# Performance work log

Measured on AMD Instinct MI355X. Metric: run time of the kernel, lower is better.

## Reference

```python
import jax, jax.numpy as jnp
import numpy as np
import math

N, S, E, H = 32, 64, 512, 4
HD = E // H
EQ = E // 4
L2_TEMP = 13.544
LN_EPS = 1e-5


def _ln(x, g, b):
    m = jnp.mean(x, -1, keepdims=True)
    v = jnp.var(x, -1, keepdims=True)
    return (x - m) * jax.lax.rsqrt(v + LN_EPS) * g + b


def setup_inputs() -> dict:
    key = jax.random.key(0)
    ks = jax.random.split(key, 16)
    sc = 0.02
    inp = {
        "x": jax.random.normal(ks[0], (N, S, E), jnp.float32),
        # MultiheadAttention params (torch layout: in_proj_weight (3E,E))
        "Wqkv": jax.random.normal(ks[1], (3 * E, E), jnp.float32) * sc,
        "bqkv": jnp.zeros((3 * E,), jnp.float32),
        "Wo": jax.random.normal(ks[2], (E, E), jnp.float32) * sc,
        "bo": jnp.zeros((E,), jnp.float32),
        # fc1 (E, 2E), fc2 (E, E)
        "W1": jax.random.normal(ks[3], (E, 2 * E), jnp.float32) * sc,
        "b1": jnp.zeros((E,), jnp.float32),
        "W2": jax.random.normal(ks[4], (E, E), jnp.float32) * sc,
        "b2": jnp.zeros((E,), jnp.float32),
        # layer norms
        "g1": jnp.ones((E,), jnp.float32), "be1": jnp.zeros((E,), jnp.float32),
        "g2": jnp.ones((E,), jnp.float32), "be2": jnp.zeros((E,), jnp.float32),
        # fc_diff1: Linear(E, E//4), Linear(E//4, 1)
        "d1W1": jax.random.normal(ks[5], (EQ, E), jnp.float32) * sc,
        "d1b1": jnp.zeros((EQ,), jnp.float32),
        "d1W2": jax.random.normal(ks[6], (1, EQ), jnp.float32) * sc,
        "d1b2": jnp.zeros((1,), jnp.float32),
        # fc_diff2
        "d2W1": jax.random.normal(ks[7], (EQ, E), jnp.float32) * sc,
        "d2b1": jnp.zeros((EQ,), jnp.float32),
        "d2W2": jax.random.normal(ks[8], (1, EQ), jnp.float32) * sc,
        "d2b2": jnp.zeros((1,), jnp.float32),
    }
    return inp


def _mha(x, Wqkv, bqkv, Wo, bo):
    n, s, e = x.shape
    qkv = x @ Wqkv.T + bqkv
    q, k, v = jnp.split(qkv, 3, axis=-1)
    sh = lambda t: t.reshape(n, s, H, HD).transpose(0, 2, 1, 3)  # (n,H,s,hd)
    q, k, v = sh(q), sh(k), sh(v)
    scores = jnp.einsum('bhqd,bhkd->bhqk', q, k) / math.sqrt(HD)
    a = jax.nn.softmax(scores, axis=-1)
    o = jnp.einsum('bhqk,bhkd->bhqd', a, v).transpose(0, 2, 1, 3).reshape(n, s, e)
    return o @ Wo.T + bo, a.mean(axis=1)  # averaged attn weights (torch default)


def _pair_mlp(diff_w, W1a, b1a, W2a, b2a):
    # F.relu applied after every 'layer' (Linear, Dropout(eval=id), Linear)
    h = jax.nn.relu(diff_w @ W1a.T + b1a)  # relu(dropout(relu)) == relu composed -> same
    return jax.nn.relu(h @ W2a.T + b2a)[..., 0]  # (N,f,f)


def reference(x, Wqkv, bqkv, Wo, bo, W1, b1, W2, b2, g1, be1, g2, be2,
              d1W1, d1b1, d1W2, d1b2, d2W1, d2b1, d2W2, d2b2):
    # diff[b,f,g,e] = x[b,g,e] - x[b,f,e]
    diff = x[:, None, :, :] - x[:, :, None, :]  # (N,f,f,E)
    x1_attn = jax.nn.softmax(-jnp.sum(diff * diff, -1) / L2_TEMP, axis=-1)  # (N,f,f)
    x1 = jnp.einsum('bfg,bge->bfe', x1_attn, x)
    x2, x2_attn = _mha(x, Wqkv, bqkv, Wo, bo)
    x_res = jnp.concatenate([x1, x2], axis=-1)
    h = x + jax.nn.relu(x_res @ W1.T + b1)  # dropout eval = identity
    h = _ln(h, g1, be1)
    h = h + jax.nn.relu(h @ W2.T + b2)
    out = _ln(h, g2, be2)
    diff1 = _pair_mlp(diff * x1_attn[..., None], d1W1, d1b1, d1W2, d1b2)
    diff2 = _pair_mlp(diff * x2_attn[..., None], d2W1, d2b1, d2W2, d2b2)
    return out, x1_attn[:, None], x2_attn[:, None], diff1, diff2
```

## Files before the change

### kernel.cpp

```cpp
#include <hip/hip_runtime.h>
#include <math.h>

#define NB 32
#define SS 64
#define EE 512
#define L2T 13.544f
#define LNEPS 1e-5f

using bf16x8 = __attribute__((ext_vector_type(8))) __bf16;
using u16x8  = __attribute__((ext_vector_type(8))) unsigned short;
using f32x4  = __attribute__((ext_vector_type(4))) float;

typedef const void __attribute__((address_space(1))) cv_global;
typedef void __attribute__((address_space(3))) v_lds;

__device__ inline unsigned short f2bf(float f) {
    union { float f; unsigned u; } v; v.f = f;
    unsigned r = v.u + 0x7fff + ((v.u >> 16) & 1);
    return (unsigned short)(r >> 16);
}
__device__ inline float bf2f(unsigned short h) {
    union { unsigned u; float f; } v; v.u = (unsigned)h << 16;
    return v.f;
}

__global__ __launch_bounds__(256)
void convert_all(const float* __restrict__ x, const float* __restrict__ Wqkv,
                 const float* __restrict__ Wo, const float* __restrict__ W1,
                 const float* __restrict__ W2, const float* __restrict__ d1,
                 const float* __restrict__ d2, unsigned short* __restrict__ dst) {
    int i = blockIdx.x * 256 + threadIdx.x;
    const float* s; int off;
    if (i < 1048576)      { s = x;    off = 0; }
    else if (i < 1835008) { s = Wqkv; off = 1048576; }
    else if (i < 2097152) { s = Wo;   off = 1835008; }
    else if (i < 2621440) { s = W1;   off = 2097152; }
    else if (i < 2883584) { s = W2;   off = 2621440; }
    else if (i < 2949120) { s = d1;   off = 2883584; }
    else                  { s = d2;   off = 2949120; }
    dst[i] = f2bf(s[i - off]);
}

__global__ __launch_bounds__(256)
void l2attn_x1(const float* __restrict__ x, float* __restrict__ x1_attn,
               unsigned short* __restrict__ x_resb) {
    const int f = blockIdx.x, b = blockIdx.y;
    const int tid = threadIdx.x, wave = tid >> 6, lane = tid & 63;
    __shared__ float d2s[64];
    __shared__ float attn_s[64];

    const float4* xb = (const float4*)(x + (size_t)b * SS * EE);
    float4 xf0 = xb[f * 128 + lane * 2];
    float4 xf1 = xb[f * 128 + lane * 2 + 1];

    for (int g = wave; g < 64; g += 4) {
        float4 a0 = xb[g * 128 + lane * 2];
        float4 a1 = xb[g * 128 + lane * 2 + 1];
        float dx, s = 0.f;
        dx = a0.x - xf0.x; s += dx * dx;
        dx = a0.y - xf0.y; s += dx * dx;
        dx = a0.z - xf0.z; s += dx * dx;
        dx = a0.w - xf0.w; s += dx * dx;
        dx = a1.x - xf1.x; s += dx * dx;
        dx = a1.y - xf1.y; s += dx * dx;
        dx = a1.z - xf1.z; s += dx * dx;
        dx = a1.w - xf1.w; s += dx * dx;
        #pragma unroll
        for (int m = 32; m; m >>= 1) s += __shfl_xor(s, m);
        if (lane == 0) d2s[g] = s;
    }
    __syncthreads();

    if (tid < 64) {
        float v = -d2s[tid] * (1.0f / L2T);
        float mx = v;
        #pragma unroll
        for (int m = 32; m; m >>= 1) mx = fmaxf(mx, __shfl_xor(mx, m));
        float e = expf(v - mx);
        float sum = e;
        #pragma unroll
        for (int m = 32; m; m >>= 1) sum += __shfl_xor(sum, m);
        float a = e / sum;
        x1_attn[((size_t)b * SS + f) * SS + tid] = a;
        attn_s[tid] = a;
    }
    __syncthreads();

    const float* xbf = x + (size_t)b * SS * EE;
    float acc0 = 0.f, acc1 = 0.f;
    #pragma unroll 8
    for (int g = 0; g < 64; ++g) {
        float ag = attn_s[g];
        acc0 += ag * xbf[g * EE + tid];
        acc1 += ag * xbf[g * EE + tid + 256];
    }
    unsigned short* dst = x_resb + ((size_t)b * SS + f) * 1024;
    dst[tid] = f2bf(acc0);
    dst[tid + 256] = f2bf(acc1);
}

template <bool RELU, bool OUTBF16>
__global__ __launch_bounds__(256)
void gemm_mfma(const unsigned short* __restrict__ A, int lda,
               const unsigned short* __restrict__ B, int ldb,
               const float* __restrict__ bias, float* __restrict__ Cf,
               unsigned short* __restrict__ Cb, int ldc, int K) {
    __shared__ unsigned short Asl[64 * 32];
    __shared__ unsigned short Bsl[64 * 32];
    const int tid = threadIdx.x;
    const int wave = tid >> 6, lane = tid & 63;
    const int m0 = blockIdx.y * 64, n0 = blockIdx.x * 64;
    const int wm = (wave >> 1) * 32, wn = (wave & 1) * 32;

    f32x4 acc00 = {0.f, 0.f, 0.f, 0.f};
    f32x4 acc01 = acc00, acc10 = acc00, acc11 = acc00;

    const int srow = tid >> 2, scol = (tid & 3) * 8;
    const unsigned short* Ag = A + (size_t)(m0 + srow) * lda + scol;
    const unsigned short* Bg = B + (size_t)(n0 + srow) * ldb + scol;
    v_lds* AslW = (v_lds*)(Asl + wave * 512);
    v_lds* BslW = (v_lds*)(Bsl + wave * 512);

    const int fr = lane & 15;
    const int kq = (lane >> 4) * 8;

    for (int k0 = 0; k0 < K; k0 += 32) {
        __builtin_amdgcn_global_load_lds((cv_global*)(Ag + k0), AslW, 16, 0, 0);
        __builtin_amdgcn_global_load_lds((cv_global*)(Bg + k0), BslW, 16, 0, 0);
        __syncthreads();
        bf16x8 a0 = *(const bf16x8*)(Asl + (wm + fr) * 32 + kq);
        bf16x8 a1 = *(const bf16x8*)(Asl + (wm + 16 + fr) * 32 + kq);
        bf16x8 b0 = *(const bf16x8*)(Bsl + (wn + fr) * 32 + kq);
        bf16x8 b1 = *(const bf16x8*)(Bsl + (wn + 16 + fr) * 32 + kq);
        acc00 = __builtin_amdgcn_mfma_f32_16x16x32_bf16(a0, b0, acc00, 0, 0, 0);
        acc01 = __builtin_amdgcn_mfma_f32_16x16x32_bf16(a0, b1, acc01, 0, 0, 0);
        acc10 = __builtin_amdgcn_mfma_f32_16x16x32_bf16(a1, b0, acc10, 0, 0, 0);
        acc11 = __builtin_amdgcn_mfma_f32_16x16x32_bf16(a1, b1, acc11, 0, 0, 0);
        __syncthreads();
    }

    const int crow = (lane >> 4) * 4, ccol = lane & 15;
    float bj0 = bias ? bias[n0 + wn + ccol] : 0.f;
    float bj1 = bias ? bias[n0 + wn + 16 + ccol] : 0.f;

    auto store_tile = [&](f32x4 acc, int mt, int nt, float bj) {
        #pragma unroll
        for (int r = 0; r < 4; ++r) {
            size_t m = (size_t)(m0 + mt + crow + r);
            int n = n0 + nt + ccol;
            float v = acc[r] + bj;
            if (RELU) v = fmaxf(v, 0.f);
            if (OUTBF16) Cb[m * ldc + n] = f2bf(v);
            else         Cf[m * ldc + n] = v;
        }
    };
    store_tile(acc00, wm,      wn,      bj0);
    store_tile(acc01, wm,      wn + 16, bj1);
    store_tile(acc10, wm + 16, wn,      bj0);
    store_tile(acc11, wm + 16, wn + 16, bj1);
}

__global__ __launch_bounds__(256)
void mha_attn(const unsigned short* __restrict__ qkv,
              unsigned short* __restrict__ o_buf, float* __restrict__ x2_attn) {
    const int hh = blockIdx.x;
    const int h = hh >> 1, half = hh & 1;
    const int b = blockIdx.y;
    const int tid = threadIdx.x, wave = tid >> 6, lane = tid & 63;

    __shared__ unsigned short Qs[32 * 136];
    __shared__ unsigned short Ks[64 * 136];
    __shared__ unsigned short Vt[128 * 72];
    __shared__ float sc[32 * 68];
    __shared__ unsigned short Pb[32 * 72];

    const unsigned short* base = qkv + (size_t)b * 64 * 1536;

    {
        int row = tid >> 3, col = (tid & 7) * 16;
        const unsigned short* src = base + (half * 32 + row) * 1536 + h * 128 + col;
        *(u16x8*)(Qs + row * 136 + col)     = *(const u16x8*)(src);
        *(u16x8*)(Qs + row * 136 + col + 8) = *(const u16x8*)(src + 8);
    }
    {
        int row = tid >> 2, col = (tid & 3) * 32;
        const unsigned short* src = base + row * 1536 + 512 + h * 128 + col;
        #pragma unroll
        for (int j = 0; j < 4; ++j)
            *(u16x8*)(Ks + row * 136 + col + j * 8) = *(const u16x8*)(src + j * 8);
    }
    {
        int g = tid >> 2, col = (tid & 3) * 32;
        const unsigned short* src = base + g * 1536 + 1024 + h * 128 + col;
        #pragma unroll
        for (int j = 0; j < 4; ++j) {
            u16x8 v = *(const u16x8*)(src + j * 8);
            #pragma unroll
            for (int e = 0; e < 8; ++e)
                Vt[(col + j * 8 + e) * 72 + g] = v[e];
        }
    }
    __syncthreads();

    const int fr = lane & 15, kq = (lane >> 4) * 8;
    const int crow = (lane >> 4) * 4, ccol = lane & 15;
    const int wm = (wave >> 1) * 16;

    {
        const int wn = (wave & 1) * 32;
        f32x4 s0 = {0.f, 0.f, 0.f, 0.f}, s1 = s0;
        #pragma unroll
        for (int k0 = 0; k0 < 128; k0 += 32) {
            bf16x8 a  = *(const bf16x8*)(Qs + (wm + fr) * 136 + k0 + kq);
            bf16x8 b0 = *(const bf16x8*)(Ks + (wn + fr) * 136 + k0 + kq);
            bf16x8 b1 = *(const bf16x8*)(Ks + (wn + 16 + fr) * 136 + k0 + kq);
            s0 = __builtin_amdgcn_mfma_f32_16x16x32_bf16(a, b0, s0, 0, 0, 0);
            s1 = __builtin_amdgcn_mfma_f32_16x16x32_bf16(a, b1, s1, 0, 0, 0);
        }
        const float scale = 0.08838834764831845f;
        #pragma unroll
        for (int r = 0; r < 4; ++r) {
            sc[(wm + crow + r) * 68 + wn + ccol]      = s0[r] * scale;
            sc[(wm + crow + r) * 68 + wn + 16 + ccol] = s1[r] * scale;
        }
    }
    __syncthreads();

    #pragma unroll
    for (int i = 0; i < 8; ++i) {
        int f = wave * 8 + i;
        float v = sc[f * 68 + lane];
        float mx = v;
        #pragma unroll
        for (int m = 32; m; m >>= 1) mx = fmaxf(mx, __shfl_xor(mx, m));
        float e = expf(v - mx);
        float sum = e;
        #pragma unroll
        for (int m = 32; m; m >>= 1) sum += __shfl_xor(sum, m);
        float a = e / sum;
        Pb[f * 72 + lane] = f2bf(a);
        atomicAdd(&x2_attn[((size_t)b * 64 + half * 32 + f) * 64 + lane], 0.25f * a);
    }
    __syncthreads();

    {
        const int wn2 = (wave & 1) * 64;
        f32x4 o[4];
        #pragma unroll
        for (int t = 0; t < 4; ++t) o[t] = f32x4{0.f, 0.f, 0.f, 0.f};
        #pragma unroll
        for (int k0 = 0; k0 < 64; k0 += 32) {
            bf16x8 a = *(const bf16x8*)(Pb + (wm + fr) * 72 + k0 + kq);
            #pragma unroll
            for (int t = 0; t < 4; ++t) {
                bf16x8 bv = *(const bf16x8*)(Vt + (wn2 + t * 16 + fr) * 72 + k0 + kq);
                o[t] = __builtin_amdgcn_mfma_f32_16x16x32_bf16(a, bv, o[t], 0, 0, 0);
            }
        }
        #pragma unroll
        for (int t = 0; t < 4; ++t) {
            #pragma unroll
            for (int r = 0; r < 4; ++r) {
                size_t m = (size_t)b * 64 + half * 32 + wm + crow + r;
                int col = h * 128 + wn2 + t * 16 + ccol;
                o_buf[m * 512 + col] = f2bf(o[t][r]);
            }
        }
    }
}

__global__ __launch_bounds__(256)
void add_ln(const float* __restrict__ base, const float* __restrict__ u,
            const float* __restrict__ gam, const float* __restrict__ bet,
            float* __restrict__ out, unsigned short* __restrict__ outb) {
    const int row = blockIdx.x;
    const int tid = threadIdx.x, wave = tid >> 6, lane = tid & 63;
    const float* br = base + (size_t)row * EE;
    const float* ur = u + (size_t)row * EE;
    float t0 = br[tid] + ur[tid];
    float t1 = br[tid + 256] + ur[tid + 256];
    float s = t0 + t1, sq = t0 * t0 + t1 * t1;
    #pragma unroll
    for (int m = 32; m; m >>= 1) {
        s += __shfl_xor(s, m);
        sq += __shfl_xor(sq, m);
    }
    __shared__ float ssum[4], ssq[4];
    if (lane == 0) { ssum[wave] = s; ssq[wave] = sq; }
    __syncthreads();
    s = ssum[0] + ssum[1] + ssum[2] + ssum[3];
    sq = ssq[0] + ssq[1] + ssq[2] + ssq[3];
    float mean = s * (1.0f / EE);
    float var = sq * (1.0f / EE) - mean * mean;
    float inv = rsqrtf(var + LNEPS);
    float v0 = (t0 - mean) * inv * gam[tid] + bet[tid];
    float v1 = (t1 - mean) * inv * gam[tid + 256] + bet[tid + 256];
    float* orow = out + (size_t)row * EE;
    orow[tid] = v0;
    orow[tid + 256] = v1;
    if (outb) {
        unsigned short* obr = outb + (size_t)row * EE;
        obr[tid] = f2bf(v0);
        obr[tid + 256] = f2bf(v1);
    }
}

__global__ __launch_bounds__(256)
void pair_mlp(const float* __restrict__ P, const float* __restrict__ a1,
              const float* __restrict__ a2, const float* __restrict__ d1b1,
              const float* __restrict__ d1w2, const float* __restrict__ d1b2,
              const float* __restrict__ d2b1, const float* __restrict__ d2w2,
              const float* __restrict__ d2b2, float* __restrict__ out1,
              float* __restrict__ out2) {
    const int f = blockIdx.x, b = blockIdx.y;
    const int tid = threadIdx.x, wave = tid >> 6, lane = tid & 63;
    const size_t row = (size_t)b * SS + f;
    const int c0 = lane * 2, c1 = lane * 2 + 1;

    const float p1f0 = P[row * 256 + c0],       p1f1 = P[row * 256 + c1];
    const float p2f0 = P[row * 256 + 128 + c0], p2f1 = P[row * 256 + 128 + c1];
    const float w10 = d1w2[c0], w11 = d1w2[c1];
    const float w20 = d2w2[c0], w21 = d2w2[c1];
    const float b10 = d1b1[c0], b11 = d1b1[c1];
    const float b20 = d2b1[c0], b21 = d2b1[c1];
    const float bb1 = d1b2[0], bb2 = d2b2[0];

    const float* a1r = a1 + row * SS;
    const float* a2r = a2 + row * SS;
    const size_t bbase = (size_t)b * SS * 256;

    for (int g = wave; g < 64; g += 4) {
        float aa1 = a1r[g], aa2 = a2r[g];
        float q10 = P[bbase + g * 256 + c0],       q11 = P[bbase + g * 256 + c1];
        float q20 = P[bbase + g * 256 + 128 + c0], q21 = P[bbase + g * 256 + 128 + c1];
        float h10 = fmaxf(aa1 * (q10 - p1f0) + b10, 0.f);
        float h11 = fmaxf(aa1 * (q11 - p1f1) + b11, 0.f);
        float h20 = fmaxf(aa2 * (q20 - p2f0) + b20, 0.f);
        float h21 = fmaxf(aa2 * (q21 - p2f1) + b21, 0.f);
        float s1 = w10 * h10 + w11 * h11;
        float s2 = w20 * h20 + w21 * h21;
        #pragma unroll
        for (int m = 32; m; m >>= 1) {
            s1 += __shfl_xor(s1, m);
            s2 += __shfl_xor(s2, m);
        }
        if (lane == 0) {
            out1[row * SS + g] = fmaxf(s1 + bb1, 0.f);
            out2[row * SS + g] = fmaxf(s2 + bb2, 0.f);
        }
    }
}

extern "C" void kernel_launch(void* const* d_in, const int* in_sizes, int n_in,
                              void* d_out, int out_size, void* d_ws,
                              size_t ws_size, hipStream_t stream) {
    const float* x    = (const float*)d_in[0];
    const float* Wqkv = (const float*)d_in[1];
    const float* bqkv = (const float*)d_in[2];
    const float* Wo   = (const float*)d_in[3];
    const float* bo   = (const float*)d_in[4];
    const float* W1   = (const float*)d_in[5];
    const float* b1   = (const float*)d_in[6];
    const float* W2   = (const float*)d_in[7];
    const float* b2   = (const float*)d_in[8];
    const float* g1   = (const float*)d_in[9];
    const float* be1  = (const float*)d_in[10];
    const float* g2   = (const float*)d_in[11];
    const float* be2  = (const float*)d_in[12];
    const float* d1W1 = (const float*)d_in[13];
    const float* d1b1 = (const float*)d_in[14];
    const float* d1W2 = (const float*)d_in[15];
    const float* d1b2 = (const float*)d_in[16];
    const float* d2W1 = (const float*)d_in[17];
    const float* d2b1 = (const float*)d_in[18];
    const float* d2W2 = (const float*)d_in[19];
    const float* d2b2 = (const float*)d_in[20];

    float* out      = (float*)d_out;
    float* out_main = out;
    float* x1_attn  = out + 1048576;
    float* x2_attn  = out + 1048576 + 131072;
    float* diff1    = out + 1048576 + 2 * 131072;
    float* diff2    = out + 1048576 + 3 * 131072;

    float* ws    = (float*)d_ws;
    float* u_buf = ws;
    float* h_buf = u_buf + 1048576;
    float* P     = h_buf + 1048576;
    unsigned short* bb    = (unsigned short*)(P + 524288);
    unsigned short* xb    = bb;
    unsigned short* Wqkvb = bb + 1048576;
    unsigned short* Wob   = bb + 1835008;
    unsigned short* W1b   = bb + 2097152;
    unsigned short* W2b   = bb + 2621440;
    unsigned short* Wpb   = bb + 2883584;
    unsigned short* qkvb  = bb + 3014656;
    unsigned short* ob    = bb + 6160384;
    unsigned short* x_resb= bb + 7208960;
    unsigned short* hb    = bb + 9306112;

    hipMemsetAsync(x2_attn, 0, 131072 * sizeof(float), stream);

    convert_all<<<11776, 256, 0, stream>>>(x, Wqkv, Wo, W1, W2, d1W1, d2W1, bb);

    l2attn_x1<<<dim3(64, 32), 256, 0, stream>>>(x, x1_attn, x_resb);

    gemm_mfma<false, true><<<dim3(24, 32), 256, 0, stream>>>(
        xb, 512, Wqkvb, 512, bqkv, nullptr, qkvb, 1536, 512);

    mha_attn<<<dim3(8, 32), 256, 0, stream>>>(qkvb, ob, x2_attn);

    gemm_mfma<false, true><<<dim3(8, 32), 256, 0, stream>>>(
        ob, 512, Wob, 512, bo, nullptr, x_resb + 512, 1024, 512);

    gemm_mfma<true, false><<<dim3(8, 32), 256, 0, stream>>>(
        x_resb, 1024, W1b, 1024, b1, u_buf, nullptr, 512, 1024);

    add_ln<<<2048, 256, 0, stream>>>(x, u_buf, g1, be1, h_buf, hb);

    gemm_mfma<true, false><<<dim3(8, 32), 256, 0, stream>>>(
        hb, 512, W2b, 512, b2, u_buf, nullptr, 512, 512);

    add_ln<<<2048, 256, 0, stream>>>(h_buf, u_buf, g2, be2, out_main, nullptr);

    gemm_mfma<false, false><<<dim3(4, 32), 256, 0, stream>>>(
        xb, 512, Wpb, 512, nullptr, P, nullptr, 256, 512);

    pair_mlp<<<dim3(64, 32), 256, 0, stream>>>(P, x1_attn, x2_attn, d1b1, d1W2,
                                               d1b2, d2b1, d2W2, d2b2, diff1,
                                               diff2);
}
```

Before: 212.3 us.

## Rework GEMM tiling with swizzled K=64 LDS, drop atomics and memset, fuse x conversion

The GEMM now loads K=64 slices into XOR-swizzled LDS, which avoids bank conflicts. Its M-tile is templated, and BM=32 doubles the block count for the small GEMMs. The x-to-bf16 conversion moves into l2attn_x1, and the weight conversion is vectorized with float4. The head-averaged attention now uses per-head plain writes, reduced later in pair_mlp, so the atomics and the memset are gone. This costs extra workspace traffic for the per-head probabilities and adds more LDS per block.

New measurement: 198.1 us. 6.7% less time.

```diff
diff --git a/kernel.cpp b/kernel.cpp
--- a/kernel.cpp
+++ b/kernel.cpp
@@ -25,37 +25,40 @@
 }
 
 __global__ __launch_bounds__(256)
-void convert_all(const float* __restrict__ x, const float* __restrict__ Wqkv,
-                 const float* __restrict__ Wo, const float* __restrict__ W1,
-                 const float* __restrict__ W2, const float* __restrict__ d1,
-                 const float* __restrict__ d2, unsigned short* __restrict__ dst) {
+void convert_w(const float* __restrict__ Wqkv, const float* __restrict__ Wo,
+               const float* __restrict__ W1, const float* __restrict__ W2,
+               const float* __restrict__ d1, const float* __restrict__ d2,
+               unsigned short* __restrict__ dst) {
     int i = blockIdx.x * 256 + threadIdx.x;
     const float* s; int off;
-    if (i < 1048576)      { s = x;    off = 0; }
-    else if (i < 1835008) { s = Wqkv; off = 1048576; }
-    else if (i < 2097152) { s = Wo;   off = 1835008; }
-    else if (i < 2621440) { s = W1;   off = 2097152; }
-    else if (i < 2883584) { s = W2;   off = 2621440; }
-    else if (i < 2949120) { s = d1;   off = 2883584; }
-    else                  { s = d2;   off = 2949120; }
-    dst[i] = f2bf(s[i - off]);
+    if (i < 196608)      { s = Wqkv; off = 0; }
+    else if (i < 262144) { s = Wo;   off = 196608; }
+    else if (i < 393216) { s = W1;   off = 262144; }
+    else if (i < 458752) { s = W2;   off = 393216; }
+    else if (i < 475136) { s = d1;   off = 458752; }
+    else                 { s = d2;   off = 475136; }
+    float4 v = ((const float4*)s)[i - off];
+    ushort4 o;
+    o.x = f2bf(v.x); o.y = f2bf(v.y); o.z = f2bf(v.z); o.w = f2bf(v.w);
+    ((ushort4*)dst)[i] = o;
 }
 
 __global__ __launch_bounds__(256)
 void l2attn_x1(const float* __restrict__ x, float* __restrict__ x1_attn,
-               unsigned short* __restrict__ x_resb) {
+               unsigned short* __restrict__ x_resb,
+               unsigned short* __restrict__ xb) {
     const int f = blockIdx.x, b = blockIdx.y;
     const int tid = threadIdx.x, wave = tid >> 6, lane = tid & 63;
     __shared__ float d2s[64];
     __shared__ float attn_s[64];
 
-    const float4* xb = (const float4*)(x + (size_t)b * SS * EE);
-    float4 xf0 = xb[f * 128 + lane * 2];
-    float4 xf1 = xb[f * 128 + lane * 2 + 1];
+    const float4* xv = (const float4*)(x + (size_t)b * SS * EE);
+    float4 xf0 = xv[f * 128 + lane * 2];
+    float4 xf1 = xv[f * 128 + lane * 2 + 1];
 
     for (int g = wave; g < 64; g += 4) {
-        float4 a0 = xb[g * 128 + lane * 2];
-        float4 a1 = xb[g * 128 + lane * 2 + 1];
+        float4 a0 = xv[g * 128 + lane * 2];
+        float4 a1 = xv[g * 128 + lane * 2 + 1];
         float dx, s = 0.f;
         dx = a0.x - xf0.x; s += dx * dx;
         dx = a0.y - xf0.y; s += dx * dx;
@@ -97,72 +100,89 @@
     unsigned short* dst = x_resb + ((size_t)b * SS + f) * 1024;
     dst[tid] = f2bf(acc0);
     dst[tid + 256] = f2bf(acc1);
-}
-
-template <bool RELU, bool OUTBF16>
+    unsigned short* xrow = xb + ((size_t)b * SS + f) * EE;
+    xrow[tid] = f2bf(xbf[f * EE + tid]);
+    xrow[tid + 256] = f2bf(xbf[f * EE + tid + 256]);
+}
+
+template <int BM, bool RELU, bool OUTBF16>
 __global__ __launch_bounds__(256)
 void gemm_mfma(const unsigned short* __restrict__ A, int lda,
                const unsigned short* __restrict__ B, int ldb,
                const float* __restrict__ bias, float* __restrict__ Cf,
                unsigned short* __restrict__ Cb, int ldc, int K) {
-    __shared__ unsigned short Asl[64 * 32];
-    __shared__ unsigned short Bsl[64 * 32];
-    const int tid = threadIdx.x;
-    const int wave = tid >> 6, lane = tid & 63;
-    const int m0 = blockIdx.y * 64, n0 = blockIdx.x * 64;
-    const int wm = (wave >> 1) * 32, wn = (wave & 1) * 32;
-
-    f32x4 acc00 = {0.f, 0.f, 0.f, 0.f};
-    f32x4 acc01 = acc00, acc10 = acc00, acc11 = acc00;
-
-    const int srow = tid >> 2, scol = (tid & 3) * 8;
-    const unsigned short* Ag = A + (size_t)(m0 + srow) * lda + scol;
-    const unsigned short* Bg = B + (size_t)(n0 + srow) * ldb + scol;
-    v_lds* AslW = (v_lds*)(Asl + wave * 512);
-    v_lds* BslW = (v_lds*)(Bsl + wave * 512);
-
+    __shared__ unsigned short Asl[BM * 64];
+    __shared__ unsigned short Bsl[64 * 64];
+    const int tid = threadIdx.x, wave = tid >> 6, lane = tid & 63;
+    const int m0 = blockIdx.y * BM, n0 = blockIdx.x * 64;
+
+    constexpr int RF = BM / 32;
+    const int wm = (wave >> 1) * (BM / 2);
+    const int wn = (wave & 1) * 32;
     const int fr = lane & 15;
-    const int kq = (lane >> 4) * 8;
-
-    for (int k0 = 0; k0 < K; k0 += 32) {
-        __builtin_amdgcn_global_load_lds((cv_global*)(Ag + k0), AslW, 16, 0, 0);
-        __builtin_amdgcn_global_load_lds((cv_global*)(Bg + k0), BslW, 16, 0, 0);
+    const int kq4 = lane >> 4;
+
+    f32x4 acc[RF][2] = {};
+
+    for (int k0 = 0; k0 < K; k0 += 64) {
+        #pragma unroll
+        for (int c0 = 0; c0 < BM * 8; c0 += 256) {
+            int cc = c0 + tid, r = cc >> 3, q = cc & 7;
+            int col = (q ^ (r & 7)) * 8;
+            __builtin_amdgcn_global_load_lds(
+                (cv_global*)(A + (size_t)(m0 + r) * lda + k0 + col),
+                (v_lds*)(Asl + c0 * 8 + wave * 512), 16, 0, 0);
+        }
+        #pragma unroll
+        for (int c0 = 0; c0 < 512; c0 += 256) {
+            int cc = c0 + tid, r = cc >> 3, q = cc & 7;
+            int col = (q ^ (r & 7)) * 8;
+            __builtin_amdgcn_global_load_lds(
+                (cv_global*)(B + (size_t)(n0 + r) * ldb + k0 + col),
+                (v_lds*)(Bsl + c0 * 8 + wave * 512), 16, 0, 0);
+        }
         __syncthreads();
-        bf16x8 a0 = *(const bf16x8*)(Asl + (wm + fr) * 32 + kq);
-        bf16x8 a1 = *(const bf16x8*)(Asl + (wm + 16 + fr) * 32 + kq);
-        bf16x8 b0 = *(const bf16x8*)(Bsl + (wn + fr) * 32 + kq);
-        bf16x8 b1 = *(const bf16x8*)(Bsl + (wn + 16 + fr) * 32 + kq);
-        acc00 = __builtin_amdgcn_mfma_f32_16x16x32_bf16(a0, b0, acc00, 0, 0, 0);
-        acc01 = __builtin_amdgcn_mfma_f32_16x16x32_bf16(a0, b1, acc01, 0, 0, 0);
-        acc10 = __builtin_amdgcn_mfma_f32_16x16x32_bf16(a1, b0, acc10, 0, 0, 0);
-        acc11 = __builtin_amdgcn_mfma_f32_16x16x32_bf16(a1, b1, acc11, 0, 0, 0);
+        #pragma unroll
+        for (int j = 0; j < 2; ++j) {
+            int kc = kq4 + j * 4;
+            int rb0 = wn + fr, rb1 = wn + 16 + fr;
+            bf16x8 b0 = *(const bf16x8*)(Bsl + rb0 * 64 + (kc ^ (rb0 & 7)) * 8);
+            bf16x8 b1 = *(const bf16x8*)(Bsl + rb1 * 64 + (kc ^ (rb1 & 7)) * 8);
+            #pragma unroll
+            for (int r = 0; r < RF; ++r) {
+                int ra = wm + r * 16 + fr;
+                bf16x8 af = *(const bf16x8*)(Asl + ra * 64 + (kc ^ (ra & 7)) * 8);
+                acc[r][0] = __builtin_amdgcn_mfma_f32_16x16x32_bf16(af, b0, acc[r][0], 0, 0, 0);
+                acc[r][1] = __builtin_amdgcn_mfma_f32_16x16x32_bf16(af, b1, acc[r][1], 0, 0, 0);
+            }
+        }
         __syncthreads();
     }
 
     const int crow = (lane >> 4) * 4, ccol = lane & 15;
     float bj0 = bias ? bias[n0 + wn + ccol] : 0.f;
     float bj1 = bias ? bias[n0 + wn + 16 + ccol] : 0.f;
-
-    auto store_tile = [&](f32x4 acc, int mt, int nt, float bj) {
-        #pragma unroll
-        for (int r = 0; r < 4; ++r) {
-            size_t m = (size_t)(m0 + mt + crow + r);
-            int n = n0 + nt + ccol;
-            float v = acc[r] + bj;
-            if (RELU) v = fmaxf(v, 0.f);
-            if (OUTBF16) Cb[m * ldc + n] = f2bf(v);
-            else         Cf[m * ldc + n] = v;
-        }
-    };
-    store_tile(acc00, wm,      wn,      bj0);
-    store_tile(acc01, wm,      wn + 16, bj1);
-    store_tile(acc10, wm + 16, wn,      bj0);
-    store_tile(acc11, wm + 16, wn + 16, bj1);
+    #pragma unroll
+    for (int r = 0; r < RF; ++r) {
+        #pragma unroll
+        for (int c = 0; c < 2; ++c) {
+            float bj = c ? bj1 : bj0;
+            #pragma unroll
+            for (int i = 0; i < 4; ++i) {
+                size_t m = (size_t)(m0 + wm + r * 16 + crow + i);
+                int n = n0 + wn + c * 16 + ccol;
+                float v = acc[r][c][i] + bj;
+                if (RELU) v = fmaxf(v, 0.f);
+                if (OUTBF16) Cb[m * ldc + n] = f2bf(v);
+                else         Cf[m * ldc + n] = v;
+            }
+        }
+    }
 }
 
 __global__ __launch_bounds__(256)
 void mha_attn(const unsigned short* __restrict__ qkv,
-              unsigned short* __restrict__ o_buf, float* __restrict__ x2_attn) {
+              unsigned short* __restrict__ o_buf, float* __restrict__ pws) {
     const int hh = blockIdx.x;
     const int h = hh >> 1, half = hh & 1;
     const int b = blockIdx.y;
@@ -239,7 +259,7 @@
         for (int m = 32; m; m >>= 1) sum += __shfl_xor(sum, m);
         float a = e / sum;
         Pb[f * 72 + lane] = f2bf(a);
-        atomicAdd(&x2_attn[((size_t)b * 64 + half * 32 + f) * 64 + lane], 0.25f * a);
+        pws[(((size_t)b * 4 + h) * 64 + half * 32 + f) * 64 + lane] = a;
     }
     __syncthreads();
 
@@ -307,11 +327,11 @@
 
 __global__ __launch_bounds__(256)
 void pair_mlp(const float* __restrict__ P, const float* __restrict__ a1,
-              const float* __restrict__ a2, const float* __restrict__ d1b1,
+              const float* __restrict__ pws, const float* __restrict__ d1b1,
               const float* __restrict__ d1w2, const float* __restrict__ d1b2,
               const float* __restrict__ d2b1, const float* __restrict__ d2w2,
-              const float* __restrict__ d2b2, float* __restrict__ out1,
-              float* __restrict__ out2) {
+              const float* __restrict__ d2b2, float* __restrict__ x2_attn,
+              float* __restrict__ out1, float* __restrict__ out2) {
     const int f = blockIdx.x, b = blockIdx.y;
     const int tid = threadIdx.x, wave = tid >> 6, lane = tid & 63;
     const size_t row = (size_t)b * SS + f;
@@ -326,11 +346,15 @@
     const float bb1 = d1b2[0], bb2 = d2b2[0];
 
     const float* a1r = a1 + row * SS;
-    const float* a2r = a2 + row * SS;
+    const float* ph0 = pws + (((size_t)b * 4 + 0) * 64 + f) * 64;
+    const float* ph1 = pws + (((size_t)b * 4 + 1) * 64 + f) * 64;
+    const float* ph2 = pws + (((size_t)b * 4 + 2) * 64 + f) * 64;
+    const float* ph3 = pws + (((size_t)b * 4 + 3) * 64 + f) * 64;
     const size_t bbase = (size_t)b * SS * 256;
 
     for (int g = wave; g < 64; g += 4) {
-        float aa1 = a1r[g], aa2 = a2r[g];
+        float aa1 = a1r[g];
+        float aa2 = 0.25f * (ph0[g] + ph1[g] + ph2[g] + ph3[g]);
         float q10 = P[bbase + g * 256 + c0],       q11 = P[bbase + g * 256 + c1];
         float q20 = P[bbase + g * 256 + 128 + c0], q21 = P[bbase + g * 256 + 128 + c1];
         float h10 = fmaxf(aa1 * (q10 - p1f0) + b10, 0.f);
@@ -345,6 +369,7 @@
             s2 += __shfl_xor(s2, m);
         }
         if (lane == 0) {
+            x2_attn[row * SS + g] = aa2;
             out1[row * SS + g] = fmaxf(s1 + bb1, 0.f);
             out2[row * SS + g] = fmaxf(s2 + bb2, 0.f);
         }
@@ -387,7 +412,8 @@
     float* u_buf = ws;
     float* h_buf = u_buf + 1048576;
     float* P     = h_buf + 1048576;
-    unsigned short* bb    = (unsigned short*)(P + 524288);
+    float* pws   = P + 524288;
+    unsigned short* bb    = (unsigned short*)(pws + 524288);
     unsigned short* xb    = bb;
     unsigned short* Wqkvb = bb + 1048576;
     unsigned short* Wob   = bb + 1835008;
@@ -399,34 +425,33 @@
     unsigned short* x_resb= bb + 7208960;
     unsigned short* hb    = bb + 9306112;
 
-    hipMemsetAsync(x2_attn, 0, 131072 * sizeof(float), stream);
-
-    convert_all<<<11776, 256, 0, stream>>>(x, Wqkv, Wo, W1, W2, d1W1, d2W1, bb);
-
-    l2attn_x1<<<dim3(64, 32), 256, 0, stream>>>(x, x1_attn, x_resb);
-
-    gemm_mfma<false, true><<<dim3(24, 32), 256, 0, stream>>>(
+    convert_w<<<1920, 256, 0, stream>>>(Wqkv, Wo, W1, W2, d1W1, d2W1,
+                                        bb + 1048576);
+
+    l2attn_x1<<<dim3(64, 32), 256, 0, stream>>>(x, x1_attn, x_resb, xb);
+
+    gemm_mfma<64, false, true><<<dim3(24, 32), 256, 0, stream>>>(
         xb, 512, Wqkvb, 512, bqkv, nullptr, qkvb, 1536, 512);
 
-    mha_attn<<<dim3(8, 32), 256, 0, stream>>>(qkvb, ob, x2_attn);
-
-    gemm_mfma<false, true><<<dim3(8, 32), 256, 0, stream>>>(
+    mha_attn<<<dim3(8, 32), 256, 0, stream>>>(qkvb, ob, pws);
+
+    gemm_mfma<32, false, true><<<dim3(8, 64), 256, 0, stream>>>(
         ob, 512, Wob, 512, bo, nullptr, x_resb + 512, 1024, 512);
 
-    gemm_mfma<true, false><<<dim3(8, 32), 256, 0, stream>>>(
+    gemm_mfma<32, true, false><<<dim3(8, 64), 256, 0, stream>>>(
         x_resb, 1024, W1b, 1024, b1, u_buf, nullptr, 512, 1024);
 
     add_ln<<<2048, 256, 0, stream>>>(x, u_buf, g1, be1, h_buf, hb);
 
-    gemm_mfma<true, false><<<dim3(8, 32), 256, 0, stream>>>(
+    gemm_mfma<32, true, false><<<dim3(8, 64), 256, 0, stream>>>(
         hb, 512, W2b, 512, b2, u_buf, nullptr, 512, 512);
 
     add_ln<<<2048, 256, 0, stream>>>(h_buf, u_buf, g2, be2, out_main, nullptr);
 
-    gemm_mfma<false, false><<<dim3(4, 32), 256, 0, stream>>>(
+    gemm_mfma<32, false, false><<<dim3(4, 64), 256, 0, stream>>>(
         xb, 512, Wpb, 512, nullptr, P, nullptr, 256, 512);
 
-    pair_mlp<<<dim3(64, 32), 256, 0, stream>>>(P, x1_attn, x2_attn, d1b1, d1W2,
-                                               d1b2, d2b1, d2W2, d2b2, diff1,
-                                               diff2);
-}
+    pair_mlp<<<dim3(64, 32), 256, 0, stream>>>(P, x1_attn, pws, d1b1, d1W2,
+                                               d1b2, d2b1, d2W2, d2b2, x2_attn,
+                                               diff1, diff2);
+}
```
